# Kernel optimization log

Hardware: AMD Instinct MI355X
Metric: run time of the kernel (lower is better)

Reference implementation:

```python
import jax, jax.numpy as jnp
import numpy as np

B_, N_, H_ = 4, 256, 32          # batch, nodes, neighbors (edges = B*N*H)
NC_IN, NC_OUT = 16, 16
NUM_FREQ, D_OUT, M_IN = 3, 3, 3  # degree_in = degree_out = 1 -> 2*1+1
EDGE_DIM, HID = 16, 64
LN_EPS = 1e-5


def _ln(x, gamma):
    # torch F.layer_norm over last dim, beta fixed at zero
    mu = jnp.mean(x, axis=-1, keepdims=True)
    var = jnp.var(x, axis=-1, keepdims=True)
    return (x - mu) * jax.lax.rsqrt(var + LN_EPS) * gamma


def setup_inputs() -> dict:
    key = jax.random.key(0)
    ks = jax.random.split(key, 8)

    def lin(k, fin, fout):
        lim = 1.0 / np.sqrt(fin)
        kw, kb = jax.random.split(k)
        W = jax.random.uniform(kw, (fin, fout), jnp.float32, -lim, lim)
        b = jax.random.uniform(kb, (fout,), jnp.float32, -lim, lim)
        return W, b

    W1, b1 = lin(ks[0], EDGE_DIM + 1, HID)
    W2, b2 = lin(ks[1], HID, HID)
    W3, b3 = lin(ks[2], HID, NUM_FREQ * NC_IN * NC_OUT)
    return {
        "feat": jax.random.normal(ks[3], (B_, N_, H_, EDGE_DIM + 1), jnp.float32),
        "basis": jax.random.normal(ks[4], (B_, N_, H_, D_OUT, M_IN, NUM_FREQ), jnp.float32),
        "W1": W1, "b1": b1, "g1": jnp.ones((HID,), jnp.float32),
        "W2": W2, "b2": b2, "g2": jnp.ones((HID,), jnp.float32),
        "W3": W3, "b3": b3,
    }


def reference(feat, basis, W1, b1, g1, W2, b2, g2, W3, b3):
    # radial MLP: Linear -> SiLU -> LN -> Linear -> SiLU -> LN -> Linear
    h = _ln(jax.nn.silu(feat @ W1 + b1), g1)
    h = _ln(jax.nn.silu(h @ W2 + b2), g2)
    r = h @ W3 + b3                                   # (b, n, k, o*i*f)
    R = r.reshape(*r.shape[:-1], NC_OUT, NC_IN, NUM_FREQ)  # '(o i f) -> o i f'
    # per-frequency multiply-accumulate: sum_f R[...,o,i,f] * B[...,d,m,f]
    out = jnp.einsum('bnkoif,bnkdmf->bnkodim', R, basis)   # (b,n,k,o,d,i,m)
    b, n, k = out.shape[:3]
    # contiguous reshape matches torch rearrange + view: (b,n,k, d_out*nc_out, nc_in*m_in)
    return out.reshape(b, n, k, NC_OUT * D_OUT, NC_IN * M_IN)
```

## Files before the change

kernel.cpp:

```cpp
#include <hip/hip_runtime.h>

#define E_TOTAL 32768
#define F_IN 17
#define HID 64
#define NJ 768

using bf16x8 = __attribute__((ext_vector_type(8))) short;
using f32x4  = __attribute__((ext_vector_type(4))) float;

__device__ __forceinline__ unsigned short f2bf(float x){
    unsigned u = __float_as_uint(x);
    u += 0x7fffu + ((u >> 16) & 1u);
    return (unsigned short)(u >> 16);
}

__global__ __launch_bounds__(256) void prep_w3(const float* __restrict__ W3,
                                               unsigned short* __restrict__ w3t){
    int t = blockIdx.x * 256 + threadIdx.x;
    int n = t >> 6, k = t & 63;
    w3t[t] = f2bf(W3[k * NJ + n]);
}

__global__ __launch_bounds__(256) void mlp_kernel(const float* __restrict__ feat,
        const float* __restrict__ W1, const float* __restrict__ b1, const float* __restrict__ g1,
        const float* __restrict__ W2, const float* __restrict__ b2, const float* __restrict__ g2,
        unsigned short* __restrict__ hb){
    __shared__ float sW1[F_IN * HID];
    __shared__ float sW2[HID * HID];
    __shared__ float sC[4 * HID];
    __shared__ float sFeat[16 * F_IN];
    __shared__ __align__(16) float sH1[16][HID];

    int tid = threadIdx.x;
    int e0  = blockIdx.x * 16;
    for (int i = tid; i < F_IN * HID; i += 256) sW1[i] = W1[i];
    for (int i = tid; i < HID * HID; i += 256) sW2[i] = W2[i];
    if (tid < 64) { sC[tid] = b1[tid]; sC[64 + tid] = g1[tid];
                    sC[128 + tid] = b2[tid]; sC[192 + tid] = g2[tid]; }
    for (int i = tid; i < 16 * F_IN; i += 256) sFeat[i] = feat[(size_t)e0 * F_IN + i];
    __syncthreads();

    int j = tid & 63, wv = tid >> 6;
    float acc[4], x[4], s1[4], s2[4];

    #pragma unroll
    for (int q = 0; q < 4; ++q) acc[q] = sC[j];
    for (int k = 0; k < F_IN; ++k){
        float w = sW1[k * 64 + j];
        #pragma unroll
        for (int q = 0; q < 4; ++q) acc[q] += sFeat[(wv * 4 + q) * F_IN + k] * w;
    }
    #pragma unroll
    for (int q = 0; q < 4; ++q){
        float a = acc[q];
        float sg = 1.0f / (1.0f + __expf(-a));
        x[q] = a * sg; s1[q] = x[q]; s2[q] = x[q] * x[q];
    }
    #pragma unroll
    for (int m = 1; m < 64; m <<= 1){
        #pragma unroll
        for (int q = 0; q < 4; ++q){
            s1[q] += __shfl_xor(s1[q], m);
            s2[q] += __shfl_xor(s2[q], m);
        }
    }
    #pragma unroll
    for (int q = 0; q < 4; ++q){
        float mu  = s1[q] * (1.0f / 64.0f);
        float var = s2[q] * (1.0f / 64.0f) - mu * mu;
        float rs  = rsqrtf(var + 1e-5f);
        sH1[wv * 4 + q][j] = (x[q] - mu) * rs * sC[64 + j];
    }

    #pragma unroll
    for (int q = 0; q < 4; ++q) acc[q] = sC[128 + j];
    for (int k4 = 0; k4 < 16; ++k4){
        float hv[4][4];
        #pragma unroll
        for (int q = 0; q < 4; ++q) *(float4*)hv[q] = *(const float4*)&sH1[wv * 4 + q][k4 * 4];
        #pragma unroll
        for (int kk = 0; kk < 4; ++kk){
            float w = sW2[(k4 * 4 + kk) * 64 + j];
            #pragma unroll
            for (int q = 0; q < 4; ++q) acc[q] += hv[q][kk] * w;
        }
    }
    #pragma unroll
    for (int q = 0; q < 4; ++q){
        float a = acc[q];
        float sg = 1.0f / (1.0f + __expf(-a));
        x[q] = a * sg; s1[q] = x[q]; s2[q] = x[q] * x[q];
    }
    #pragma unroll
    for (int m = 1; m < 64; m <<= 1){
        #pragma unroll
        for (int q = 0; q < 4; ++q){
            s1[q] += __shfl_xor(s1[q], m);
            s2[q] += __shfl_xor(s2[q], m);
        }
    }
    #pragma unroll
    for (int q = 0; q < 4; ++q){
        float mu  = s1[q] * (1.0f / 64.0f);
        float var = s2[q] * (1.0f / 64.0f) - mu * mu;
        float rs  = rsqrtf(var + 1e-5f);
        float h2  = (x[q] - mu) * rs * sC[192 + j];
        hb[(size_t)(e0 + wv * 4 + q) * 64 + j] = f2bf(h2);
    }
}

__global__ __launch_bounds__(256) void tp_kernel(const unsigned short* __restrict__ hb,
        const unsigned short* __restrict__ w3t, const float* __restrict__ b3,
        const float* __restrict__ basis, float* __restrict__ out){
    __shared__ __align__(16) unsigned short sA[16 * 72];
    __shared__ float sB3[NJ];
    __shared__ float sBasis[16 * 27];
    __shared__ float sR[16 * 776];

    int tid = threadIdx.x;
    int bid = blockIdx.x;
    int e0  = bid * 16;

    for (int idx = tid; idx < 512; idx += 256){
        int e = idx >> 5, c = idx & 31;
        unsigned v = ((const unsigned*)(hb + (size_t)e0 * 64))[idx];
        *((unsigned*)(sA + e * 72 + c * 2)) = v;
    }
    for (int idx = tid; idx < NJ; idx += 256) sB3[idx] = b3[idx];
    for (int idx = tid; idx < 16 * 27; idx += 256) sBasis[idx] = basis[(size_t)e0 * 27 + idx];
    __syncthreads();

    int wv = tid >> 6, l = tid & 63;
    int col = l & 15, kg = l >> 4;

    bf16x8 a0 = *(const bf16x8*)(sA + (l & 15) * 72 + kg * 8);
    bf16x8 a1 = *(const bf16x8*)(sA + (l & 15) * 72 + 32 + kg * 8);
    #pragma unroll 3
    for (int t = 0; t < 12; ++t){
        int n0 = wv * 192 + t * 16;
        bf16x8 bb0 = *(const bf16x8*)(w3t + (size_t)(n0 + col) * 64 + kg * 8);
        bf16x8 bb1 = *(const bf16x8*)(w3t + (size_t)(n0 + col) * 64 + 32 + kg * 8);
        f32x4 acc = {0.f, 0.f, 0.f, 0.f};
        acc = __builtin_amdgcn_mfma_f32_16x16x32_bf16(a0, bb0, acc, 0, 0, 0);
        acc = __builtin_amdgcn_mfma_f32_16x16x32_bf16(a1, bb1, acc, 0, 0, 0);
        float bj = sB3[n0 + col];
        #pragma unroll
        for (int r = 0; r < 4; ++r){
            int e = kg * 4 + r;
            sR[e * 776 + n0 + col] = acc[r] + bj;
        }
    }
    __syncthreads();

    int g = l >> 4, s = l & 15;
    int e_loc = wv * 4 + g;
    float bs[27];
    #pragma unroll
    for (int z = 0; z < 27; ++z) bs[z] = sBasis[e_loc * 27 + z];
    float* outE = out + (size_t)(e0 + e_loc) * 2304;
    const float* Rrow = sR + e_loc * 776;

    #pragma unroll 4
    for (int task = 0; task < 16; ++task){
        int oi = task * 16 + s;
        float r0 = Rrow[oi * 3 + 0];
        float r1 = Rrow[oi * 3 + 1];
        float r2 = Rrow[oi * 3 + 2];
        #pragma unroll
        for (int d = 0; d < 3; ++d){
            float* p = outE + task * 144 + d * 48 + s * 3;
            #pragma unroll
            for (int m = 0; m < 3; ++m){
                int z = d * 9 + m * 3;
                p[m] = r0 * bs[z + 0] + r1 * bs[z + 1] + r2 * bs[z + 2];
            }
        }
    }
}

extern "C" void kernel_launch(void* const* d_in, const int* in_sizes, int n_in,
                              void* d_out, int out_size, void* d_ws, size_t ws_size,
                              hipStream_t stream) {
    const float* feat  = (const float*)d_in[0];
    const float* basis = (const float*)d_in[1];
    const float* W1 = (const float*)d_in[2];
    const float* b1 = (const float*)d_in[3];
    const float* g1 = (const float*)d_in[4];
    const float* W2 = (const float*)d_in[5];
    const float* b2 = (const float*)d_in[6];
    const float* g2 = (const float*)d_in[7];
    const float* W3 = (const float*)d_in[8];
    const float* b3 = (const float*)d_in[9];
    float* out = (float*)d_out;

    unsigned short* hbuf = (unsigned short*)d_ws;
    unsigned short* w3t  = hbuf + (size_t)E_TOTAL * HID;

    prep_w3<<<NJ * HID / 256, 256, 0, stream>>>(W3, w3t);
    mlp_kernel<<<E_TOTAL / 16, 256, 0, stream>>>(feat, W1, b1, g1, W2, b2, g2, hbuf);
    tp_kernel<<<E_TOTAL / 16, 256, 0, stream>>>(hbuf, w3t, b3, basis, out);
}
```

Baseline: 389.7 us.

## Chunk tensor-product kernel to shrink LDS footprint and raise occupancy

```diff
diff --git a/kernel.cpp b/kernel.cpp
--- a/kernel.cpp
+++ b/kernel.cpp
@@ -109,72 +109,65 @@
     }
 }
 
-__global__ __launch_bounds__(256) void tp_kernel(const unsigned short* __restrict__ hb,
+__global__ __launch_bounds__(256, 4) void tp_kernel(const unsigned short* __restrict__ hb,
         const unsigned short* __restrict__ w3t, const float* __restrict__ b3,
         const float* __restrict__ basis, float* __restrict__ out){
-    __shared__ __align__(16) unsigned short sA[16 * 72];
-    __shared__ float sB3[NJ];
-    __shared__ float sBasis[16 * 27];
-    __shared__ float sR[16 * 776];
+    __shared__ __align__(16) float sR[16 * 194];
 
     int tid = threadIdx.x;
-    int bid = blockIdx.x;
-    int e0  = bid * 16;
-
-    for (int idx = tid; idx < 512; idx += 256){
-        int e = idx >> 5, c = idx & 31;
-        unsigned v = ((const unsigned*)(hb + (size_t)e0 * 64))[idx];
-        *((unsigned*)(sA + e * 72 + c * 2)) = v;
-    }
-    for (int idx = tid; idx < NJ; idx += 256) sB3[idx] = b3[idx];
-    for (int idx = tid; idx < 16 * 27; idx += 256) sBasis[idx] = basis[(size_t)e0 * 27 + idx];
-    __syncthreads();
+    int e0  = blockIdx.x * 16;
 
     int wv = tid >> 6, l = tid & 63;
     int col = l & 15, kg = l >> 4;
 
-    bf16x8 a0 = *(const bf16x8*)(sA + (l & 15) * 72 + kg * 8);
-    bf16x8 a1 = *(const bf16x8*)(sA + (l & 15) * 72 + 32 + kg * 8);
-    #pragma unroll 3
-    for (int t = 0; t < 12; ++t){
-        int n0 = wv * 192 + t * 16;
-        bf16x8 bb0 = *(const bf16x8*)(w3t + (size_t)(n0 + col) * 64 + kg * 8);
-        bf16x8 bb1 = *(const bf16x8*)(w3t + (size_t)(n0 + col) * 64 + 32 + kg * 8);
-        f32x4 acc = {0.f, 0.f, 0.f, 0.f};
-        acc = __builtin_amdgcn_mfma_f32_16x16x32_bf16(a0, bb0, acc, 0, 0, 0);
-        acc = __builtin_amdgcn_mfma_f32_16x16x32_bf16(a1, bb1, acc, 0, 0, 0);
-        float bj = sB3[n0 + col];
+    const unsigned short* hrow = hb + (size_t)(e0 + col) * 64;
+    bf16x8 a0 = *(const bf16x8*)(hrow + kg * 8);
+    bf16x8 a1 = *(const bf16x8*)(hrow + 32 + kg * 8);
+
+    int e_loc = wv * 4 + kg;
+    int s     = col;
+    float bs[27];
+    const float* bp = basis + (size_t)(e0 + e_loc) * 27;
+    #pragma unroll
+    for (int z = 0; z < 27; ++z) bs[z] = bp[z];
+    float* outE = out + (size_t)(e0 + e_loc) * 2304;
+    const float* Rrow = sR + e_loc * 194;
+
+    for (int c4 = 0; c4 < 4; ++c4){
         #pragma unroll
-        for (int r = 0; r < 4; ++r){
-            int e = kg * 4 + r;
-            sR[e * 776 + n0 + col] = acc[r] + bj;
-        }
-    }
-    __syncthreads();
-
-    int g = l >> 4, s = l & 15;
-    int e_loc = wv * 4 + g;
-    float bs[27];
-    #pragma unroll
-    for (int z = 0; z < 27; ++z) bs[z] = sBasis[e_loc * 27 + z];
-    float* outE = out + (size_t)(e0 + e_loc) * 2304;
-    const float* Rrow = sR + e_loc * 776;
-
-    #pragma unroll 4
-    for (int task = 0; task < 16; ++task){
-        int oi = task * 16 + s;
-        float r0 = Rrow[oi * 3 + 0];
-        float r1 = Rrow[oi * 3 + 1];
-        float r2 = Rrow[oi * 3 + 2];
-        #pragma unroll
-        for (int d = 0; d < 3; ++d){
-            float* p = outE + task * 144 + d * 48 + s * 3;
+        for (int t = 0; t < 3; ++t){
+            int n0 = c4 * 192 + wv * 48 + t * 16;
+            const unsigned short* wrow = w3t + (size_t)(n0 + col) * 64;
+            bf16x8 bb0 = *(const bf16x8*)(wrow + kg * 8);
+            bf16x8 bb1 = *(const bf16x8*)(wrow + 32 + kg * 8);
+            f32x4 acc = {0.f, 0.f, 0.f, 0.f};
+            acc = __builtin_amdgcn_mfma_f32_16x16x32_bf16(a0, bb0, acc, 0, 0, 0);
+            acc = __builtin_amdgcn_mfma_f32_16x16x32_bf16(a1, bb1, acc, 0, 0, 0);
+            float bj = b3[n0 + col];
+            int cL = wv * 48 + t * 16 + col;
             #pragma unroll
-            for (int m = 0; m < 3; ++m){
-                int z = d * 9 + m * 3;
-                p[m] = r0 * bs[z + 0] + r1 * bs[z + 1] + r2 * bs[z + 2];
+            for (int r = 0; r < 4; ++r){
+                int e = kg * 4 + r;
+                sR[e * 194 + cL] = acc[r] + bj;
             }
         }
+        __syncthreads();
+
+        #pragma unroll
+        for (int t2 = 0; t2 < 4; ++t2){
+            int o = c4 * 4 + t2;
+            const float* rp = Rrow + t2 * 48 + s * 3;
+            float r0 = rp[0], r1 = rp[1], r2 = rp[2];
+            #pragma unroll
+            for (int d = 0; d < 3; ++d){
+                float* p = outE + o * 144 + d * 48 + s * 3;
+                int z = d * 9;
+                p[0] = r0 * bs[z + 0] + r1 * bs[z + 1] + r2 * bs[z + 2];
+                p[1] = r0 * bs[z + 3] + r1 * bs[z + 4] + r2 * bs[z + 5];
+                p[2] = r0 * bs[z + 6] + r1 * bs[z + 7] + r2 * bs[z + 8];
+            }
+        }
+        __syncthreads();
     }
 }
 
```

Result: faster. 363.7 us (-6.7%).
